# Kernel tuning notes

Measured on AMD Instinct MI355X. Metric: run time of the kernel, lower is better.

## Reference

```python
import jax, jax.numpy as jnp
import numpy as np


def setup_inputs() -> dict:
    key = jax.random.key(0)
    ks = jax.random.split(key, 16)
    s = 0.02
    return {
        "video": jax.random.normal(ks[0], (256, 10, 7, 7, 512), jnp.float32),
        "audio": jax.random.normal(ks[1], (10, 256, 128), jnp.float32),
        "Wv1": jax.random.normal(ks[2], (512, 512), jnp.float32) * s,
        "bv1": jnp.zeros((512,), jnp.float32),
        "Wa1": jax.random.normal(ks[3], (512, 128), jnp.float32) * s,
        "ba1": jnp.zeros((512,), jnp.float32),
        "Wb": jax.random.normal(ks[4], (256, 512), jnp.float32) * s,
        "bb": jnp.zeros((256,), jnp.float32),
        "Wc": jax.random.normal(ks[5], (512, 256), jnp.float32) * s,
        "bc": jnp.zeros((512,), jnp.float32),
        "Wv2": jax.random.normal(ks[6], (256, 512), jnp.float32) * s,
        "bv2": jnp.zeros((256,), jnp.float32),
        "Wa2": jax.random.normal(ks[7], (256, 128), jnp.float32) * s,
        "ba2": jnp.zeros((256,), jnp.float32),
        "Ws": jax.random.normal(ks[8], (1, 256), jnp.float32) * s,
        "bs": jnp.zeros((1,), jnp.float32),
    }


def reference(video, audio, Wv1, bv1, Wa1, ba1, Wb, bb, Wc, bc, Wv2, bv2, Wa2, ba2, Ws, bs):
    # video: [B, T, H, W, 512]; audio: [T, B, 128] (transposed inside, as in torch code)
    relu = jax.nn.relu
    audio = jnp.transpose(audio, (1, 0, 2))                  # [B, T, 128]
    B, T, H, W, Vd = video.shape
    BT, HW = B * T, H * W
    af = audio.reshape(BT, -1)                               # [BT, 128]
    vf = video.reshape(B, T, HW, Vd)                         # raw visual feature

    # channel attention
    aq1 = relu(af @ Wa1.T + ba1)[:, None, :]                 # [BT, 1, 512]
    vq1 = relu(vf @ Wv1.T + bv1).reshape(BT, HW, -1)         # [BT, 49, 512]
    avq = jnp.mean(aq1 * vq1, axis=-2)                       # [BT, 512]
    avq = relu(avq @ Wb.T + bb)                              # [BT, 256]
    c_att_maps = jax.nn.sigmoid(avq @ Wc.T + bc).reshape(B, T, 1, Vd)
    c_att = (vf * (c_att_maps + 1.0)).reshape(BT, HW, Vd)    # [BT, 49, 512]

    # spatial attention
    cq = relu(c_att @ Wv2.T + bv2)                           # [BT, 49, 256]
    aq2 = relu(af @ Wa2.T + ba2)[:, None, :]                 # [BT, 1, 256]
    logits = jnp.tanh((cq * aq2) @ Ws.T + bs)                # [BT, 49, 1]
    s_att = jax.nn.softmax(jnp.transpose(logits, (0, 2, 1)), axis=-1)  # [BT, 1, 49]

    out = jnp.matmul(s_att, c_att)                           # [BT, 1, 512]
    return out.reshape(B, T, Vd)
```

## Files before the change

### kernel.cpp

```cpp
#include <hip/hip_runtime.h>

typedef __bf16 bf16x8 __attribute__((ext_vector_type(8)));
typedef float f32x4 __attribute__((ext_vector_type(4)));

__device__ __forceinline__ unsigned short f2bf(float f) {
    union { float f; unsigned int u; } x; x.f = f;
    unsigned int r = x.u + 0x7FFFu + ((x.u >> 16) & 1u);
    return (unsigned short)(r >> 16);
}
__device__ __forceinline__ float bf2f(unsigned short v) {
    union { unsigned int u; float f; } x; x.u = ((unsigned int)v) << 16; return x.f;
}
__device__ __forceinline__ float bf2f_lo(unsigned int w) {
    union { unsigned int u; float f; } x; x.u = w << 16; return x.f;
}
__device__ __forceinline__ float bf2f_hi(unsigned int w) {
    union { unsigned int u; float f; } x; x.u = w & 0xffff0000u; return x.f;
}
__device__ __forceinline__ unsigned int cvt_pk_bf16(float lo, float hi) {
    unsigned int r;
    asm("v_cvt_pk_bf16_f32 %0, %1, %2" : "=v"(r) : "v"(lo), "v"(hi));
    return r;
}
__device__ __forceinline__ void async16(const void* g, void* l) {
    __builtin_amdgcn_global_load_lds(
        (const __attribute__((address_space(1))) unsigned int*)g,
        (__attribute__((address_space(3))) unsigned int*)l, 16, 0, 0);
}

__global__ __launch_bounds__(256) void k_front(
    const float* __restrict__ video, unsigned short* __restrict__ vbf,
    const float* __restrict__ Wv1, const float* __restrict__ Wv2,
    unsigned short* __restrict__ Wv1bf, unsigned short* __restrict__ Wv2bf,
    const float* __restrict__ audio,
    const float* __restrict__ Wa1, const float* __restrict__ ba1,
    const float* __restrict__ Wa2, const float* __restrict__ ba2,
    float* __restrict__ aq1, float* __restrict__ aq2)
{
    const int b = blockIdx.x;
    const int tid = threadIdx.x;
    if (b < 4096) {
        const size_t stride = (size_t)4096 * 256;
        for (size_t c = (size_t)b * 256 + tid; c < 8028160u; c += stride) {
            const float* p = video + c * 8;
            float4 a = *(const float4*)p;
            float4 bb4 = *(const float4*)(p + 4);
            uint4 o;
            o.x = cvt_pk_bf16(a.x, a.y); o.y = cvt_pk_bf16(a.z, a.w);
            o.z = cvt_pk_bf16(bb4.x, bb4.y); o.w = cvt_pk_bf16(bb4.z, bb4.w);
            *(uint4*)(vbf + c * 8) = o;
        }
        return;
    }
    if (b < 4480) {
        int base = (b - 4096) * 1024 + tid;
#pragma unroll
        for (int r = 0; r < 4; ++r) {
            int idx = base + r * 256;
            if (idx < 262144) Wv1bf[idx] = f2bf(Wv1[idx]);
            else              Wv2bf[idx - 262144] = f2bf(Wv2[idx - 262144]);
        }
        return;
    }
    __shared__ float afs[4][128];
    const int btBase = (b - 4480) * 4;
    for (int i = tid; i < 512; i += 256) {
        int g = i >> 7, k = i & 127;
        int bt = btBase + g;
        int bb_ = bt / 10, t = bt - bb_ * 10;
        afs[g][k] = audio[(t * 256 + bb_) * 128 + k];
    }
    __syncthreads();
    const int c = tid;
    float a1a[4] = {0.f,0.f,0.f,0.f}, a1b[4] = {0.f,0.f,0.f,0.f}, a2[4] = {0.f,0.f,0.f,0.f};
    const float* w1a = Wa1 + c * 128;
    const float* w1b = Wa1 + (c + 256) * 128;
    const float* w2p = Wa2 + c * 128;
    for (int kk = 0; kk < 32; ++kk) {
        float4 va = *(const float4*)(w1a + kk * 4);
        float4 vb = *(const float4*)(w1b + kk * 4);
        float4 vc = *(const float4*)(w2p + kk * 4);
        float fa[4] = {va.x, va.y, va.z, va.w};
        float fb[4] = {vb.x, vb.y, vb.z, vb.w};
        float fc[4] = {vc.x, vc.y, vc.z, vc.w};
#pragma unroll
        for (int j = 0; j < 4; ++j) {
            int k = kk * 4 + j;
#pragma unroll
            for (int g = 0; g < 4; ++g) {
                float a = afs[g][k];
                a1a[g] += a * fa[j];
                a1b[g] += a * fb[j];
                a2[g]  += a * fc[j];
            }
        }
    }
    float b1a = ba1[c], b1b = ba1[c + 256], b2 = ba2[c];
#pragma unroll
    for (int g = 0; g < 4; ++g) {
        int bt = btBase + g;
        aq1[bt * 512 + c]       = fmaxf(a1a[g] + b1a, 0.f);
        aq1[bt * 512 + c + 256] = fmaxf(a1b[g] + b1b, 0.f);
        aq2[bt * 256 + c]       = fmaxf(a2[g] + b2, 0.f);
    }
}

__global__ __launch_bounds__(512) void k_chanatt_g(
    const unsigned short* __restrict__ videobf,
    const unsigned short* __restrict__ Wv1bf, const float* __restrict__ bv1,
    const float* __restrict__ aq1, float* __restrict__ avq)
{
    __shared__ unsigned short lds[2 * 12288];
    const int tid = threadIdx.x;
    const int wave = tid >> 6, lane = tid & 63, quad = lane >> 4, l16 = lane & 15;
    const int wm = wave >> 2, wn = wave & 3;
    const int mb = blockIdx.x >> 1, nb = blockIdx.x & 1;
    const int bt0 = mb * 2;

    auto stage = [&](int buf, int kt) {
        const int base = buf * 12288;
        {
            int row = tid >> 2, c = tid & 3;
            int hw = row & 63, btl = row >> 6;
            if (hw < 49) {
                async16(videobf + (size_t)(bt0 + btl) * 25088 + hw * 512
                                + kt * 32 + ((c ^ (row & 3)) << 3),
                        &lds[base + tid * 8]);
            }
        }
#pragma unroll
        for (int rep = 0; rep < 2; ++rep) {
            int q = tid + rep * 512;
            int row = q >> 2, c = q & 3;
            async16(Wv1bf + (size_t)((nb << 8) + row) * 512
                          + kt * 32 + ((c ^ (row & 3)) << 3),
                    &lds[base + 4096 + q * 8]);
        }
    };

    f32x4 acc[4][4];
#pragma unroll
    for (int mt = 0; mt < 4; ++mt)
#pragma unroll
        for (int nt = 0; nt < 4; ++nt)
            acc[mt][nt] = (f32x4){0.f, 0.f, 0.f, 0.f};

    stage(0, 0);
    __syncthreads();

    for (int kt = 0; kt < 16; ++kt) {
        int cur = kt & 1;
        if (kt < 15) stage(cur ^ 1, kt + 1);
        const int cb = cur * 12288;
        bf16x8 af[4];
#pragma unroll
        for (int mt = 0; mt < 4; ++mt) {
            int row = wm * 64 + mt * 16 + l16;
            af[mt] = *(const bf16x8*)&lds[cb + row * 32 + ((quad ^ (row & 3)) << 3)];
        }
#pragma unroll
        for (int nt = 0; nt < 4; ++nt) {
            int rowb = wn * 64 + nt * 16 + l16;
            bf16x8 bfr = *(const bf16x8*)&lds[cb + 4096 + rowb * 32 + ((quad ^ (rowb & 3)) << 3)];
#pragma unroll
            for (int mt = 0; mt < 4; ++mt)
                acc[mt][nt] = __builtin_amdgcn_mfma_f32_16x16x32_bf16(
                    af[mt], bfr, acc[mt][nt], 0, 0, 0);
        }
        __syncthreads();
    }

    const int bt = bt0 + wm;
#pragma unroll
    for (int nt = 0; nt < 4; ++nt) {
        int n = nb * 256 + wn * 64 + nt * 16 + l16;
        float bias = bv1[n];
        float s = 0.f;
#pragma unroll
        for (int mt = 0; mt < 4; ++mt)
#pragma unroll
            for (int r = 0; r < 4; ++r)
                if (mt < 3 || (quad == 0 && r == 0))
                    s += fmaxf(acc[mt][nt][r] + bias, 0.f);
        s += __shfl_xor(s, 16, 64);
        s += __shfl_xor(s, 32, 64);
        if (quad == 0) {
            avq[bt * 512 + n] = aq1[bt * 512 + n] * (s * (1.f / 49.f));
        }
    }
}

__global__ __launch_bounds__(256) void k_mlp(
    const float* __restrict__ avq,
    const float* __restrict__ Wb, const float* __restrict__ bb,
    const float* __restrict__ Wc, const float* __restrict__ bc,
    float* __restrict__ cmul)
{
    __shared__ float av[4][512];
    __shared__ float hid[4][256];
    const int btBase = blockIdx.x * 4;
    const int tid = threadIdx.x;
    for (int i = tid; i < 2048; i += 256) {
        int g = i >> 9, c = i & 511;
        av[g][c] = avq[(btBase + g) * 512 + c];
    }
    __syncthreads();
    {
        float a[4] = {0.f,0.f,0.f,0.f};
        const float* wrow = Wb + tid * 512;
        for (int kk = 0; kk < 128; ++kk) {
            float4 v = *(const float4*)(wrow + kk * 4);
            float w[4] = {v.x, v.y, v.z, v.w};
#pragma unroll
            for (int j = 0; j < 4; ++j)
#pragma unroll
                for (int g = 0; g < 4; ++g)
                    a[g] += av[g][kk * 4 + j] * w[j];
        }
        float bias = bb[tid];
#pragma unroll
        for (int g = 0; g < 4; ++g) hid[g][tid] = fmaxf(a[g] + bias, 0.f);
    }
    __syncthreads();
#pragma unroll
    for (int rep = 0; rep < 2; ++rep) {
        int c = tid + rep * 256;
        float a[4] = {0.f,0.f,0.f,0.f};
        const float* wrow = Wc + c * 256;
        for (int kk = 0; kk < 64; ++kk) {
            float4 v = *(const float4*)(wrow + kk * 4);
            float w[4] = {v.x, v.y, v.z, v.w};
#pragma unroll
            for (int j = 0; j < 4; ++j)
#pragma unroll
                for (int g = 0; g < 4; ++g)
                    a[g] += hid[g][kk * 4 + j] * w[j];
        }
        float bias = bc[c];
#pragma unroll
        for (int g = 0; g < 4; ++g) {
            float s = 1.f / (1.f + __expf(-(a[g] + bias)));
            cmul[(btBase + g) * 512 + c] = 1.f + s;
        }
    }
}

__global__ __launch_bounds__(512) void k_sgemm(
    const unsigned short* __restrict__ videobf,
    const float* __restrict__ cmul, const float* __restrict__ aq2,
    const unsigned short* __restrict__ Wv2bf, const float* __restrict__ bv2,
    const float* __restrict__ Wsp, const float* __restrict__ bsp,
    float* __restrict__ out)
{
    __shared__ unsigned short lds[2 * 12288];
    __shared__ float zsh[8][64];
    __shared__ float smloc[2][64];
    const int tid = threadIdx.x;
    const int wave = tid >> 6, lane = tid & 63, quad = lane >> 4, l16 = lane & 15;
    const int wm = wave >> 2, wn = wave & 3;
    const int bt0 = blockIdx.x * 2;

    const int arow = tid >> 2, ac = tid & 3;
    const int ahw = arow & 63, abtl = arow >> 6;
    const bool aok = (ahw < 49);
    const int aswz = (ac ^ (arow & 3)) << 3;
    const unsigned short* avsrc = videobf + (size_t)(bt0 + abtl) * 25088 + ahw * 512;
    const float* acm = cmul + (bt0 + abtl) * 512;
    uint4 vreg;
    float4 c0reg, c1reg;

    auto aload = [&](int kt) {
        if (aok) {
            int k0 = kt * 32 + aswz;
            vreg  = *(const uint4*)(avsrc + k0);
            c0reg = *(const float4*)(acm + k0);
            c1reg = *(const float4*)(acm + k0 + 4);
        }
    };
    auto awrite = [&](int buf) {
        if (aok) {
            uint4 o;
            o.x = cvt_pk_bf16(bf2f_lo(vreg.x) * c0reg.x, bf2f_hi(vreg.x) * c0reg.y);
            o.y = cvt_pk_bf16(bf2f_lo(vreg.y) * c0reg.z, bf2f_hi(vreg.y) * c0reg.w);
            o.z = cvt_pk_bf16(bf2f_lo(vreg.z) * c1reg.x, bf2f_hi(vreg.z) * c1reg.y);
            o.w = cvt_pk_bf16(bf2f_lo(vreg.w) * c1reg.z, bf2f_hi(vreg.w) * c1reg.w);
            *(uint4*)&lds[buf * 12288 + tid * 8] = o;
        }
    };
    auto stageB = [&](int buf, int kt) {
#pragma unroll
        for (int rep = 0; rep < 2; ++rep) {
            int q = tid + rep * 512;
            int row = q >> 2, c = q & 3;
            async16(Wv2bf + (size_t)row * 512 + kt * 32 + ((c ^ (row & 3)) << 3),
                    &lds[buf * 12288 + 4096 + q * 8]);
        }
    };

    f32x4 acc[4][4];
#pragma unroll
    for (int mt = 0; mt < 4; ++mt)
#pragma unroll
        for (int nt = 0; nt < 4; ++nt)
            acc[mt][nt] = (f32x4){0.f, 0.f, 0.f, 0.f};

    aload(0);
    stageB(0, 0);
    awrite(0);
    __syncthreads();

    for (int kt = 0; kt < 16; ++kt) {
        int cur = kt & 1;
        if (kt < 15) { aload(kt + 1); stageB(cur ^ 1, kt + 1); }
        const int cb = cur * 12288;
        bf16x8 af[4];
#pragma unroll
        for (int mt = 0; mt < 4; ++mt) {
            int row = wm * 64 + mt * 16 + l16;
            af[mt] = *(const bf16x8*)&lds[cb + row * 32 + ((quad ^ (row & 3)) << 3)];
        }
#pragma unroll
        for (int nt = 0; nt < 4; ++nt) {
            int rowb = wn * 64 + nt * 16 + l16;
            bf16x8 bfr = *(const bf16x8*)&lds[cb + 4096 + rowb * 32 + ((quad ^ (rowb & 3)) << 3)];
#pragma unroll
            for (int mt = 0; mt < 4; ++mt)
                acc[mt][nt] = __builtin_amdgcn_mfma_f32_16x16x32_bf16(
                    af[mt], bfr, acc[mt][nt], 0, 0, 0);
        }
        if (kt < 15) awrite(cur ^ 1);
        __syncthreads();
    }

    const int bt = bt0 + wm;
    float zp[16];
#pragma unroll
    for (int i = 0; i < 16; ++i) zp[i] = 0.f;
#pragma unroll
    for (int nt = 0; nt < 4; ++nt) {
        int n = wn * 64 + nt * 16 + l16;
        float bias = bv2[n];
        float co = aq2[bt * 256 + n] * Wsp[n];
#pragma unroll
        for (int mt = 0; mt < 4; ++mt)
#pragma unroll
            for (int r = 0; r < 4; ++r)
                zp[mt * 4 + r] += fmaxf(acc[mt][nt][r] + bias, 0.f) * co;
    }
#pragma unroll
    for (int i = 0; i < 16; ++i) {
        float v = zp[i];
        v += __shfl_xor(v, 1, 64);
        v += __shfl_xor(v, 2, 64);
        v += __shfl_xor(v, 4, 64);
        v += __shfl_xor(v, 8, 64);
        zp[i] = v;
    }
    if (l16 == 0) {
#pragma unroll
        for (int mt = 0; mt < 4; ++mt)
#pragma unroll
            for (int r = 0; r < 4; ++r)
                zsh[wave][mt * 16 + quad * 4 + r] = zp[mt * 4 + r];
    }
    __syncthreads();

    if (wn == 0) {
        int hw = lane;
        float z = zsh[wm * 4 + 0][hw] + zsh[wm * 4 + 1][hw]
                + zsh[wm * 4 + 2][hw] + zsh[wm * 4 + 3][hw] + bsp[0];
        float t = tanhf(z);
        float v = (hw < 49) ? t : -1e30f;
#pragma unroll
        for (int off = 32; off; off >>= 1) v = fmaxf(v, __shfl_xor(v, off, 64));
        float e = (hw < 49) ? __expf(t - v) : 0.f;
        float se = e;
#pragma unroll
        for (int off = 32; off; off >>= 1) se += __shfl_xor(se, off, 64);
        smloc[wm][hw] = (hw < 49) ? (e / se) : 0.f;
    }
    __syncthreads();

    {
        int g = tid >> 2, part = tid & 3;
        int btl = g >> 6, cg = g & 63;
        const unsigned short* vs = videobf + (size_t)(bt0 + btl) * 25088 + cg * 8;
        float s[8];
#pragma unroll
        for (int j = 0; j < 8; ++j) s[j] = 0.f;
        for (int hw = part; hw < 49; hw += 4) {
            float w = smloc[btl][hw];
            uint4 v = *(const uint4*)(vs + hw * 512);
            s[0] += w * bf2f_lo(v.x); s[1] += w * bf2f_hi(v.x);
            s[2] += w * bf2f_lo(v.y); s[3] += w * bf2f_hi(v.y);
            s[4] += w * bf2f_lo(v.z); s[5] += w * bf2f_hi(v.z);
            s[6] += w * bf2f_lo(v.w); s[7] += w * bf2f_hi(v.w);
        }
#pragma unroll
        for (int j = 0; j < 8; ++j) {
            s[j] += __shfl_xor(s[j], 1, 64);
            s[j] += __shfl_xor(s[j], 2, 64);
        }
        if (part == 0) {
            const float* cm = cmul + (bt0 + btl) * 512 + cg * 8;
            float4 m0 = *(const float4*)cm;
            float4 m1 = *(const float4*)(cm + 4);
            float mm[8] = {m0.x, m0.y, m0.z, m0.w, m1.x, m1.y, m1.z, m1.w};
            float* op = out + (bt0 + btl) * 512 + cg * 8;
#pragma unroll
            for (int j = 0; j < 8; ++j) op[j] = s[j] * mm[j];
        }
    }
}

__global__ __launch_bounds__(256) void k_prep(
    const float* __restrict__ Wv1, const float* __restrict__ Wv2,
    unsigned short* __restrict__ Wv1bf, unsigned short* __restrict__ Wv2bf)
{
    int idx = blockIdx.x * 256 + threadIdx.x;
    if (idx < 262144) {
        Wv1bf[idx] = f2bf(Wv1[idx]);
    } else {
        int j = idx - 262144;
        Wv2bf[j] = f2bf(Wv2[j]);
    }
}

__global__ __launch_bounds__(256) void k_audio(
    const float* __restrict__ audio,
    const float* __restrict__ Wa1, const float* __restrict__ ba1,
    const float* __restrict__ Wa2, const float* __restrict__ ba2,
    float* __restrict__ aq1, float* __restrict__ aq2)
{
    __shared__ float afs[4][128];
    const int btBase = blockIdx.x * 4;
    const int tid = threadIdx.x;
    for (int i = tid; i < 512; i += 256) {
        int g = i >> 7, k = i & 127;
        int bt = btBase + g;
        int b = bt / 10, t = bt - b * 10;
        afs[g][k] = audio[(t * 256 + b) * 128 + k];
    }
    __syncthreads();
    const int c = tid;
    float a1a[4] = {0.f,0.f,0.f,0.f}, a1b[4] = {0.f,0.f,0.f,0.f}, a2[4] = {0.f,0.f,0.f,0.f};
    const float* w1a = Wa1 + c * 128;
    const float* w1b = Wa1 + (c + 256) * 128;
    const float* w2p = Wa2 + c * 128;
    for (int kk = 0; kk < 32; ++kk) {
        float4 va = *(const float4*)(w1a + kk * 4);
        float4 vb = *(const float4*)(w1b + kk * 4);
        float4 vc = *(const float4*)(w2p + kk * 4);
        float fa[4] = {va.x, va.y, va.z, va.w};
        float fb[4] = {vb.x, vb.y, vb.z, vb.w};
        float fc[4] = {vc.x, vc.y, vc.z, vc.w};
#pragma unroll
        for (int j = 0; j < 4; ++j) {
            int k = kk * 4 + j;
#pragma unroll
            for (int g = 0; g < 4; ++g) {
                float a = afs[g][k];
                a1a[g] += a * fa[j];
                a1b[g] += a * fb[j];
                a2[g]  += a * fc[j];
            }
        }
    }
    float b1a = ba1[c], b1b = ba1[c + 256], b2 = ba2[c];
#pragma unroll
    for (int g = 0; g < 4; ++g) {
        int bt = btBase + g;
        aq1[bt * 512 + c]       = fmaxf(a1a[g] + b1a, 0.f);
        aq1[bt * 512 + c + 256] = fmaxf(a1b[g] + b1b, 0.f);
        aq2[bt * 256 + c]       = fmaxf(a2[g] + b2, 0.f);
    }
}

__global__ __launch_bounds__(256) void k_chanatt_fb(
    const float* __restrict__ video,
    const unsigned short* __restrict__ Wv1bf, const float* __restrict__ bv1,
    const float* __restrict__ aq1, float* __restrict__ avq)
{
    __shared__ unsigned short At[49 * 512];
    const int bt = blockIdx.x;
    const int tid = threadIdx.x;
    const int wave = tid >> 6, lane = tid & 63, quad = lane >> 4, l16 = lane & 15;
    const float* vsrc = video + (size_t)bt * 25088;

    for (int c = tid; c < 3136; c += 256) {
        int row = c >> 6, ch = c & 63;
        float4 a = *(const float4*)(vsrc + row * 512 + ch * 8);
        float4 b = *(const float4*)(vsrc + row * 512 + ch * 8 + 4);
        float f[8] = {a.x, a.y, a.z, a.w, b.x, b.y, b.z, b.w};
        unsigned int o[8];
#pragma unroll
        for (int j = 0; j < 8; ++j) o[j] = f2bf(f[j]);
        uint4 pack;
        pack.x = o[0] | (o[1] << 16); pack.y = o[2] | (o[3] << 16);
        pack.z = o[4] | (o[5] << 16); pack.w = o[6] | (o[7] << 16);
        int chs = ch ^ (row & 7);
        *(uint4*)(&At[row * 512 + chs * 8]) = pack;
    }
    __syncthreads();

    f32x4 acc[4][8];
#pragma unroll
    for (int mt = 0; mt < 4; ++mt)
#pragma unroll
        for (int nt = 0; nt < 8; ++nt)
            acc[mt][nt] = (f32x4){0.f, 0.f, 0.f, 0.f};

    for (int kk = 0; kk < 16; ++kk) {
        int chunk = kk * 4 + quad;
        bf16x8 afrag[4];
#pragma unroll
        for (int mt = 0; mt < 4; ++mt) {
            int m = ((mt == 3) ? 33 : mt * 16) + l16;
            int chs = chunk ^ (m & 7);
            afrag[mt] = *(const bf16x8*)(&At[m * 512 + chs * 8]);
        }
        int koff = chunk * 8;
#pragma unroll
        for (int nt = 0; nt < 8; ++nt) {
            int n = (wave * 8 + nt) * 16 + l16;
            bf16x8 bfrag = *(const bf16x8*)(Wv1bf + n * 512 + koff);
#pragma unroll
            for (int mt = 0; mt < 4; ++mt)
                acc[mt][nt] = __builtin_amdgcn_mfma_f32_16x16x32_bf16(
                    afrag[mt], bfrag, acc[mt][nt], 0, 0, 0);
        }
    }

#pragma unroll
    for (int nt = 0; nt < 8; ++nt) {
        int n = (wave * 8 + nt) * 16 + l16;
        float bias = bv1[n];
        float s = 0.f;
#pragma unroll
        for (int mt = 0; mt < 4; ++mt)
#pragma unroll
            for (int r = 0; r < 4; ++r)
                if (mt < 3 || (quad == 3 && r == 3))
                    s += fmaxf(acc[mt][nt][r] + bias, 0.f);
        s += __shfl_xor(s, 16, 64);
        s += __shfl_xor(s, 32, 64);
        if (quad == 0) {
            float vm = s * (1.f / 49.f);
            avq[bt * 512 + n] = aq1[bt * 512 + n] * vm;
        }
    }
}

__global__ __launch_bounds__(256) void k_spatial_fb(
    const float* __restrict__ video,
    const float* __restrict__ cmul, const float* __restrict__ aq2,
    const unsigned short* __restrict__ Wv2bf, const float* __restrict__ bv2,
    const float* __restrict__ Wsp, const float* __restrict__ bsp,
    float* __restrict__ out)
{
    __shared__ unsigned short Ct[49 * 512];
    __shared__ float w2[256];
    __shared__ float zbuf[4][64];
    __shared__ float smwl[64];
    const int bt = blockIdx.x;
    const int tid = threadIdx.x;
    const int wave = tid >> 6, lane = tid & 63, quad = lane >> 4, l16 = lane & 15;
    const float* vsrc = video + (size_t)bt * 25088;
    const float* cm = cmul + bt * 512;

    for (int c = tid; c < 3136; c += 256) {
        int row = c >> 6, ch = c & 63;
        float4 a = *(const float4*)(vsrc + row * 512 + ch * 8);
        float4 b = *(const float4*)(vsrc + row * 512 + ch * 8 + 4);
        float f[8] = {a.x, a.y, a.z, a.w, b.x, b.y, b.z, b.w};
        float4 m0 = *(const float4*)(cm + ch * 8);
        float4 m1 = *(const float4*)(cm + ch * 8 + 4);
        float mm[8] = {m0.x, m0.y, m0.z, m0.w, m1.x, m1.y, m1.z, m1.w};
        unsigned int o[8];
#pragma unroll
        for (int j = 0; j < 8; ++j) o[j] = f2bf(f[j] * mm[j]);
        uint4 pack;
        pack.x = o[0] | (o[1] << 16); pack.y = o[2] | (o[3] << 16);
        pack.z = o[4] | (o[5] << 16); pack.w = o[6] | (o[7] << 16);
        int chs = ch ^ (row & 7);
        *(uint4*)(&Ct[row * 512 + chs * 8]) = pack;
    }
    w2[tid] = aq2[bt * 256 + tid] * Wsp[tid];
    if (lane >= 49) zbuf[wave][lane] = 0.f;
    __syncthreads();

    f32x4 acc[4][4];
#pragma unroll
    for (int mt = 0; mt < 4; ++mt)
#pragma unroll
        for (int nt = 0; nt < 4; ++nt)
            acc[mt][nt] = (f32x4){0.f, 0.f, 0.f, 0.f};

    for (int kk = 0; kk < 16; ++kk) {
        int chunk = kk * 4 + quad;
        bf16x8 afrag[4];
#pragma unroll
        for (int mt = 0; mt < 4; ++mt) {
            int m = ((mt == 3) ? 33 : mt * 16) + l16;
            int chs = chunk ^ (m & 7);
            afrag[mt] = *(const bf16x8*)(&Ct[m * 512 + chs * 8]);
        }
        int koff = chunk * 8;
#pragma unroll
        for (int nt = 0; nt < 4; ++nt) {
            int n = (wave * 4 + nt) * 16 + l16;
            bf16x8 bfrag = *(const bf16x8*)(Wv2bf + n * 512 + koff);
#pragma unroll
            for (int mt = 0; mt < 4; ++mt)
                acc[mt][nt] = __builtin_amdgcn_mfma_f32_16x16x32_bf16(
                    afrag[mt], bfrag, acc[mt][nt], 0, 0, 0);
        }
    }

    float zp[16];
#pragma unroll
    for (int i = 0; i < 16; ++i) zp[i] = 0.f;
#pragma unroll
    for (int nt = 0; nt < 4; ++nt) {
        int n = (wave * 4 + nt) * 16 + l16;
        float bias = bv2[n];
        float wnc = w2[n];
#pragma unroll
        for (int mt = 0; mt < 4; ++mt)
#pragma unroll
            for (int r = 0; r < 4; ++r)
                zp[mt * 4 + r] += fmaxf(acc[mt][nt][r] + bias, 0.f) * wnc;
    }
#pragma unroll
    for (int i = 0; i < 16; ++i) {
        float v = zp[i];
        v += __shfl_xor(v, 1, 64);
        v += __shfl_xor(v, 2, 64);
        v += __shfl_xor(v, 4, 64);
        v += __shfl_xor(v, 8, 64);
        zp[i] = v;
    }
    if (l16 == 0) {
#pragma unroll
        for (int mt = 0; mt < 4; ++mt)
#pragma unroll
            for (int r = 0; r < 4; ++r)
                if (mt < 3 || (quad == 3 && r == 3)) {
                    int row = ((mt == 3) ? 33 : mt * 16) + quad * 4 + r;
                    zbuf[wave][row] = zp[mt * 4 + r];
                }
    }
    __syncthreads();

    if (wave == 0) {
        int hw = lane;
        float z = zbuf[0][hw] + zbuf[1][hw] + zbuf[2][hw] + zbuf[3][hw] + bsp[0];
        float t = tanhf(z);
        float v = (hw < 49) ? t : -1e30f;
#pragma unroll
        for (int off = 32; off; off >>= 1) v = fmaxf(v, __shfl_xor(v, off, 64));
        float e = (hw < 49) ? __expf(t - v) : 0.f;
        float se = e;
#pragma unroll
        for (int off = 32; off; off >>= 1) se += __shfl_xor(se, off, 64);
        smwl[hw] = e / se;
    }
    __syncthreads();

#pragma unroll
    for (int rep = 0; rep < 2; ++rep) {
        int cidx = tid + rep * 256;
        int chb = cidx >> 3, jj = cidx & 7;
        float s = 0.f;
        for (int hw = 0; hw < 49; ++hw) {
            int chs = chb ^ (hw & 7);
            s += smwl[hw] * bf2f(Ct[hw * 512 + chs * 8 + jj]);
        }
        out[bt * 512 + cidx] = s;
    }
}

extern "C" void kernel_launch(void* const* d_in, const int* in_sizes, int n_in,
                              void* d_out, int out_size, void* d_ws, size_t ws_size,
                              hipStream_t stream) {
    const float* video = (const float*)d_in[0];
    const float* audio = (const float*)d_in[1];
    const float* Wv1 = (const float*)d_in[2];
    const float* bv1 = (const float*)d_in[3];
    const float* Wa1 = (const float*)d_in[4];
    const float* ba1 = (const float*)d_in[5];
    const float* Wb  = (const float*)d_in[6];
    const float* bb  = (const float*)d_in[7];
    const float* Wc  = (const float*)d_in[8];
    const float* bc  = (const float*)d_in[9];
    const float* Wv2 = (const float*)d_in[10];
    const float* bv2 = (const float*)d_in[11];
    const float* Wa2 = (const float*)d_in[12];
    const float* ba2 = (const float*)d_in[13];
    const float* Wsp = (const float*)d_in[14];
    const float* bsp = (const float*)d_in[15];
    float* out = (float*)d_out;

    const size_t NEED = 147587072u;
    if (ws_size >= NEED) {
        unsigned short* videobf = (unsigned short*)d_ws;
        unsigned short* Wv1bf = videobf + 64225280;
        unsigned short* Wv2bf = Wv1bf + 262144;
        float* fbase = (float*)(Wv2bf + 131072);
        float* aq1  = fbase;
        float* aq2  = aq1 + 1310720;
        float* avq  = aq2 + 655360;
        float* cmul = avq + 1310720;

        k_front<<<5120, 256, 0, stream>>>(video, videobf, Wv1, Wv2, Wv1bf, Wv2bf,
                                          audio, Wa1, ba1, Wa2, ba2, aq1, aq2);
        k_chanatt_g<<<2560, 512, 0, stream>>>(videobf, Wv1bf, bv1, aq1, avq);
        k_mlp<<<640, 256, 0, stream>>>(avq, Wb, bb, Wc, bc, cmul);
        k_sgemm<<<1280, 512, 0, stream>>>(videobf, cmul, aq2, Wv2bf, bv2, Wsp, bsp, out);
    } else {
        float* ws = (float*)d_ws;
        float* aq1  = ws;
        float* aq2  = aq1 + 1310720;
        float* avq  = aq2 + 655360;
        float* cmul = avq + 1310720;
        unsigned short* Wv1bf = (unsigned short*)(cmul + 1310720);
        unsigned short* Wv2bf = Wv1bf + 262144;

        k_prep<<<1536, 256, 0, stream>>>(Wv1, Wv2, Wv1bf, Wv2bf);
        k_audio<<<640, 256, 0, stream>>>(audio, Wa1, ba1, Wa2, ba2, aq1, aq2);
        k_chanatt_fb<<<2560, 256, 0, stream>>>(video, Wv1bf, bv1, aq1, avq);
        k_mlp<<<640, 256, 0, stream>>>(avq, Wb, bb, Wc, bc, cmul);
        k_spatial_fb<<<2560, 256, 0, stream>>>(video, cmul, aq2, Wv2bf, bv2, Wsp, bsp, out);
    }
}
```

Measured before the change: 739.5 us.

## Fuse video fp32-to-bf16 conversion into GEMM kernels, dropping the bf16 copy

Removes the separate pass that converted the whole video tensor to bf16 in workspace. The channel-attention and spatial GEMM kernels now load fp32 video directly, convert in registers and write bf16 to LDS, and the final weighted sum reads fp32. This avoids writing and re-reading a large bf16 buffer but doubles the bytes each downstream kernel reads from video. It also replaces async global-to-LDS loads with register staging in the channel-attention kernel.

```diff
diff --git a/kernel.cpp b/kernel.cpp
--- a/kernel.cpp
+++ b/kernel.cpp
@@ -11,12 +11,6 @@
 __device__ __forceinline__ float bf2f(unsigned short v) {
     union { unsigned int u; float f; } x; x.u = ((unsigned int)v) << 16; return x.f;
 }
-__device__ __forceinline__ float bf2f_lo(unsigned int w) {
-    union { unsigned int u; float f; } x; x.u = w << 16; return x.f;
-}
-__device__ __forceinline__ float bf2f_hi(unsigned int w) {
-    union { unsigned int u; float f; } x; x.u = w & 0xffff0000u; return x.f;
-}
 __device__ __forceinline__ unsigned int cvt_pk_bf16(float lo, float hi) {
     unsigned int r;
     asm("v_cvt_pk_bf16_f32 %0, %1, %2" : "=v"(r) : "v"(lo), "v"(hi));
@@ -29,7 +23,6 @@
 }
 
 __global__ __launch_bounds__(256) void k_front(
-    const float* __restrict__ video, unsigned short* __restrict__ vbf,
     const float* __restrict__ Wv1, const float* __restrict__ Wv2,
     unsigned short* __restrict__ Wv1bf, unsigned short* __restrict__ Wv2bf,
     const float* __restrict__ audio,
@@ -39,21 +32,8 @@
 {
     const int b = blockIdx.x;
     const int tid = threadIdx.x;
-    if (b < 4096) {
-        const size_t stride = (size_t)4096 * 256;
-        for (size_t c = (size_t)b * 256 + tid; c < 8028160u; c += stride) {
-            const float* p = video + c * 8;
-            float4 a = *(const float4*)p;
-            float4 bb4 = *(const float4*)(p + 4);
-            uint4 o;
-            o.x = cvt_pk_bf16(a.x, a.y); o.y = cvt_pk_bf16(a.z, a.w);
-            o.z = cvt_pk_bf16(bb4.x, bb4.y); o.w = cvt_pk_bf16(bb4.z, bb4.w);
-            *(uint4*)(vbf + c * 8) = o;
-        }
-        return;
-    }
-    if (b < 4480) {
-        int base = (b - 4096) * 1024 + tid;
+    if (b < 384) {
+        int base = b * 1024 + tid;
 #pragma unroll
         for (int r = 0; r < 4; ++r) {
             int idx = base + r * 256;
@@ -63,7 +43,7 @@
         return;
     }
     __shared__ float afs[4][128];
-    const int btBase = (b - 4480) * 4;
+    const int btBase = (b - 384) * 4;
     for (int i = tid; i < 512; i += 256) {
         int g = i >> 7, k = i & 127;
         int bt = btBase + g;
@@ -106,7 +86,7 @@
 }
 
 __global__ __launch_bounds__(512) void k_chanatt_g(
-    const unsigned short* __restrict__ videobf,
+    const float* __restrict__ video,
     const unsigned short* __restrict__ Wv1bf, const float* __restrict__ bv1,
     const float* __restrict__ aq1, float* __restrict__ avq)
 {
@@ -117,24 +97,36 @@
     const int mb = blockIdx.x >> 1, nb = blockIdx.x & 1;
     const int bt0 = mb * 2;
 
-    auto stage = [&](int buf, int kt) {
-        const int base = buf * 12288;
-        {
-            int row = tid >> 2, c = tid & 3;
-            int hw = row & 63, btl = row >> 6;
-            if (hw < 49) {
-                async16(videobf + (size_t)(bt0 + btl) * 25088 + hw * 512
-                                + kt * 32 + ((c ^ (row & 3)) << 3),
-                        &lds[base + tid * 8]);
-            }
-        }
+    const int arow = tid >> 2, ac = tid & 3;
+    const int ahw = arow & 63, abtl = arow >> 6;
+    const bool aok = (ahw < 49);
+    const int aswz = (ac ^ (arow & 3)) << 3;
+    const float* avsrc = video + (size_t)(bt0 + abtl) * 25088 + ahw * 512;
+    float4 va, vb;
+
+    auto aload = [&](int kt) {
+        if (aok) {
+            int k0 = kt * 32 + aswz;
+            va = *(const float4*)(avsrc + k0);
+            vb = *(const float4*)(avsrc + k0 + 4);
+        }
+    };
+    auto awrite = [&](int buf) {
+        if (aok) {
+            uint4 o;
+            o.x = cvt_pk_bf16(va.x, va.y); o.y = cvt_pk_bf16(va.z, va.w);
+            o.z = cvt_pk_bf16(vb.x, vb.y); o.w = cvt_pk_bf16(vb.z, vb.w);
+            *(uint4*)&lds[buf * 12288 + tid * 8] = o;
+        }
+    };
+    auto stageB = [&](int buf, int kt) {
 #pragma unroll
         for (int rep = 0; rep < 2; ++rep) {
             int q = tid + rep * 512;
             int row = q >> 2, c = q & 3;
             async16(Wv1bf + (size_t)((nb << 8) + row) * 512
                           + kt * 32 + ((c ^ (row & 3)) << 3),
-                    &lds[base + 4096 + q * 8]);
+                    &lds[buf * 12288 + 4096 + q * 8]);
         }
     };
 
@@ -145,12 +137,14 @@
         for (int nt = 0; nt < 4; ++nt)
             acc[mt][nt] = (f32x4){0.f, 0.f, 0.f, 0.f};
 
-    stage(0, 0);
+    aload(0);
+    stageB(0, 0);
+    awrite(0);
     __syncthreads();
 
     for (int kt = 0; kt < 16; ++kt) {
         int cur = kt & 1;
-        if (kt < 15) stage(cur ^ 1, kt + 1);
+        if (kt < 15) { aload(kt + 1); stageB(cur ^ 1, kt + 1); }
         const int cb = cur * 12288;
         bf16x8 af[4];
 #pragma unroll
@@ -167,6 +161,7 @@
                 acc[mt][nt] = __builtin_amdgcn_mfma_f32_16x16x32_bf16(
                     af[mt], bfr, acc[mt][nt], 0, 0, 0);
         }
+        if (kt < 15) awrite(cur ^ 1);
         __syncthreads();
     }
 
@@ -246,7 +241,7 @@
 }
 
 __global__ __launch_bounds__(512) void k_sgemm(
-    const unsigned short* __restrict__ videobf,
+    const float* __restrict__ video,
     const float* __restrict__ cmul, const float* __restrict__ aq2,
     const unsigned short* __restrict__ Wv2bf, const float* __restrict__ bv2,
     const float* __restrict__ Wsp, const float* __restrict__ bsp,
@@ -264,15 +259,16 @@
     const int ahw = arow & 63, abtl = arow >> 6;
     const bool aok = (ahw < 49);
     const int aswz = (ac ^ (arow & 3)) << 3;
-    const unsigned short* avsrc = videobf + (size_t)(bt0 + abtl) * 25088 + ahw * 512;
+    const float* avsrc = video + (size_t)(bt0 + abtl) * 25088 + ahw * 512;
     const float* acm = cmul + (bt0 + abtl) * 512;
-    uint4 vreg;
+    float4 va, vb;
     float4 c0reg, c1reg;
 
     auto aload = [&](int kt) {
         if (aok) {
             int k0 = kt * 32 + aswz;
-            vreg  = *(const uint4*)(avsrc + k0);
+            va = *(const float4*)(avsrc + k0);
+            vb = *(const float4*)(avsrc + k0 + 4);
             c0reg = *(const float4*)(acm + k0);
             c1reg = *(const float4*)(acm + k0 + 4);
         }
@@ -280,10 +276,10 @@
     auto awrite = [&](int buf) {
         if (aok) {
             uint4 o;
-            o.x = cvt_pk_bf16(bf2f_lo(vreg.x) * c0reg.x, bf2f_hi(vreg.x) * c0reg.y);
-            o.y = cvt_pk_bf16(bf2f_lo(vreg.y) * c0reg.z, bf2f_hi(vreg.y) * c0reg.w);
-            o.z = cvt_pk_bf16(bf2f_lo(vreg.z) * c1reg.x, bf2f_hi(vreg.z) * c1reg.y);
-            o.w = cvt_pk_bf16(bf2f_lo(vreg.w) * c1reg.z, bf2f_hi(vreg.w) * c1reg.w);
+            o.x = cvt_pk_bf16(va.x * c0reg.x, va.y * c0reg.y);
+            o.y = cvt_pk_bf16(va.z * c0reg.z, va.w * c0reg.w);
+            o.z = cvt_pk_bf16(vb.x * c1reg.x, vb.y * c1reg.y);
+            o.w = cvt_pk_bf16(vb.z * c1reg.z, vb.w * c1reg.w);
             *(uint4*)&lds[buf * 12288 + tid * 8] = o;
         }
     };
@@ -384,17 +380,18 @@
     {
         int g = tid >> 2, part = tid & 3;
         int btl = g >> 6, cg = g & 63;
-        const unsigned short* vs = videobf + (size_t)(bt0 + btl) * 25088 + cg * 8;
+        const float* vs = video + (size_t)(bt0 + btl) * 25088 + cg * 8;
         float s[8];
 #pragma unroll
         for (int j = 0; j < 8; ++j) s[j] = 0.f;
         for (int hw = part; hw < 49; hw += 4) {
             float w = smloc[btl][hw];
-            uint4 v = *(const uint4*)(vs + hw * 512);
-            s[0] += w * bf2f_lo(v.x); s[1] += w * bf2f_hi(v.x);
-            s[2] += w * bf2f_lo(v.y); s[3] += w * bf2f_hi(v.y);
-            s[4] += w * bf2f_lo(v.z); s[5] += w * bf2f_hi(v.z);
-            s[6] += w * bf2f_lo(v.w); s[7] += w * bf2f_hi(v.w);
+            float4 v0 = *(const float4*)(vs + hw * 512);
+            float4 v1 = *(const float4*)(vs + hw * 512 + 4);
+            s[0] += w * v0.x; s[1] += w * v0.y;
+            s[2] += w * v0.z; s[3] += w * v0.w;
+            s[4] += w * v1.x; s[5] += w * v1.y;
+            s[6] += w * v1.z; s[7] += w * v1.w;
         }
 #pragma unroll
         for (int j = 0; j < 8; ++j) {
@@ -701,10 +698,9 @@
     const float* bsp = (const float*)d_in[15];
     float* out = (float*)d_out;
 
-    const size_t NEED = 147587072u;
+    const size_t NEED = 19136512u;
     if (ws_size >= NEED) {
-        unsigned short* videobf = (unsigned short*)d_ws;
-        unsigned short* Wv1bf = videobf + 64225280;
+        unsigned short* Wv1bf = (unsigned short*)d_ws;
         unsigned short* Wv2bf = Wv1bf + 262144;
         float* fbase = (float*)(Wv2bf + 131072);
         float* aq1  = fbase;
@@ -712,11 +708,11 @@
         float* avq  = aq2 + 655360;
         float* cmul = avq + 1310720;
 
-        k_front<<<5120, 256, 0, stream>>>(video, videobf, Wv1, Wv2, Wv1bf, Wv2bf,
+        k_front<<<1024, 256, 0, stream>>>(Wv1, Wv2, Wv1bf, Wv2bf,
                                           audio, Wa1, ba1, Wa2, ba2, aq1, aq2);
-        k_chanatt_g<<<2560, 512, 0, stream>>>(videobf, Wv1bf, bv1, aq1, avq);
+        k_chanatt_g<<<2560, 512, 0, stream>>>(video, Wv1bf, bv1, aq1, avq);
         k_mlp<<<640, 256, 0, stream>>>(avq, Wb, bb, Wc, bc, cmul);
-        k_sgemm<<<1280, 512, 0, stream>>>(videobf, cmul, aq2, Wv2bf, bv2, Wsp, bsp, out);
+        k_sgemm<<<1280, 512, 0, stream>>>(video, cmul, aq2, Wv2bf, bv2, Wsp, bsp, out);
     } else {
         float* ws = (float*)d_ws;
         float* aq1  = ws;
```

After: 712.2 us. 1.04x faster.
